# Optimization experiments

Measured on AMD Instinct MI355X. Metric: run time of the kernel, lower is better.

Reference implementation:

```python
import math
import jax, jax.numpy as jnp
import numpy as np

B, T, C = 2, 2048, 1024
H = 16
HD = C // H
WIN = 33
HALF = WIN // 2
CAUSAL = True
RADIUS, OMEGA, KSPR, STEP = 6.0, 1.0, 1.0, 0.1
EPS = 1e-8


def _spiral_step(x):
    # x: (..., 3) — the stacked (q, k, v) axis; D=3 -> rotate (x0, x1) pair.
    r = jnp.maximum(jnp.linalg.norm(x, axis=-1, keepdims=True), EPS)
    radial = (RADIUS - r) * (x / r)
    c = jnp.float32(math.cos(OMEGA * STEP))
    s = jnp.float32(math.sin(OMEGA * STEP))
    xi, xj, xl = x[..., 0], x[..., 1], x[..., 2]
    y = jnp.stack([c * xi - s * xj, s * xi + c * xj, xl], axis=-1)
    return x + STEP * (y - x + KSPR * radial)


def setup_inputs() -> dict:
    key = jax.random.key(0)
    ks = jax.random.split(key, 3)
    x = jax.random.normal(ks[0], (B, T, C), dtype=jnp.float32)
    W_attn = jax.random.normal(ks[1], (C, 3 * C), dtype=jnp.float32) * (1.0 / math.sqrt(C))
    W_proj = jax.random.normal(ks[2], (C, C), dtype=jnp.float32) * (1.0 / math.sqrt(C))
    sinks = jnp.zeros((H,), dtype=jnp.float32)
    ln_scale = jnp.ones((1,), dtype=jnp.float32) * 0.9
    ln_delta = jnp.ones((C,), dtype=jnp.float32)
    ln_bias = jnp.zeros((C,), dtype=jnp.float32)
    return {"x": x, "W_attn": W_attn, "W_proj": W_proj, "sinks": sinks,
            "ln_scale": ln_scale, "ln_delta": ln_delta, "ln_bias": ln_bias}


def reference(x, W_attn, W_proj, sinks, ln_scale, ln_delta, ln_bias):
    qkv = x @ W_attn                              # (B,T,3C)
    q, k, v = jnp.split(qkv, 3, axis=-1)          # each (B,T,C)

    # SpiralMix over the stacked (q,k,v) axis, loop_iters=2. Only q,k are
    # taken from the mixed output (v stays the pre-spiral value), matching src.
    s = jnp.stack([q, k, v], axis=-1)             # (B,T,C,3)
    s = _spiral_step(_spiral_step(s))
    q, k = s[..., 0], s[..., 1]

    def to_heads(t):
        return t.reshape(B, T, H, HD).transpose(0, 2, 1, 3)  # (B,H,T,hd)
    q, k, v = to_heads(q), to_heads(k), to_heads(v)

    # local window index
    t_idx = jnp.arange(T)
    offs = jnp.arange(-HALF, HALF + 1)
    neigh = t_idx[:, None] + offs[None, :]                    # (T,W)
    valid = (neigh >= 0) & (neigh < T)
    if CAUSAL:
        valid &= neigh <= t_idx[:, None]
    neigh_c = jnp.clip(neigh, 0, T - 1)

    k_n = k[:, :, neigh_c, :]                                 # (B,H,T,W,hd)
    v_n = v[:, :, neigh_c, :]

    inv_sqrt_d = 1.0 / math.sqrt(HD)
    scores = jnp.einsum('bhtd,bhtwd->bhtw',
                        q.astype(jnp.float32), k_n.astype(jnp.float32)) * inv_sqrt_d
    scores = jnp.where(valid[None, None], scores, -jnp.inf)

    # softmax with learned sink logits per head
    sinks_b = sinks.reshape(1, H, 1, 1).astype(scores.dtype)
    m = jnp.max(scores, axis=-1, keepdims=True)
    mj = jnp.maximum(m, sinks_b)
    exp_s = jnp.exp(scores - mj)
    denom = jnp.sum(exp_s, axis=-1, keepdims=True) + jnp.exp(sinks_b - mj)
    att = exp_s / denom                                       # (B,H,T,W)

    y = jnp.einsum('bhtw,bhtwd->bhtd', att, v_n.astype(att.dtype))
    y = y.transpose(0, 2, 1, 3).reshape(B, T, C).astype(x.dtype)
    y = y @ W_proj
    y = jnp.tanh(ln_scale * y)
    return ln_delta * y + ln_bias
```

## Files before the change

kernel.cpp:

```cpp
#include <hip/hip_runtime.h>
#include <hip/hip_fp16.h>
#include <math.h>

#define T_DIM 2048
#define B_DIM 2
#define C_DIM 1024
#define H_DIM 16
#define M_DIM 4096

typedef _Float16 f16x8 __attribute__((ext_vector_type(8)));
typedef _Float16 f16x4 __attribute__((ext_vector_type(4)));
typedef _Float16 f16x2 __attribute__((ext_vector_type(2)));
typedef float    f32x4 __attribute__((ext_vector_type(4)));

union f16x8_u { f16x8 v; f16x2 h[4]; _Float16 e[8]; };

#if defined(__has_builtin)
#  if __has_builtin(__builtin_amdgcn_fdot2)
#    define HAVE_FDOT2 1
#  endif
#endif

static __device__ __forceinline__ float FDOT2(f16x2 a, f16x2 b, float c)
{
#ifdef HAVE_FDOT2
    return __builtin_amdgcn_fdot2(a, b, c, false);
#else
    return c + (float)a[0] * (float)b[0] + (float)a[1] * (float)b[1];
#endif
}

#define ASYNC_COPY16(gsrc, ldst) \
  __builtin_amdgcn_global_load_lds( \
    (__attribute__((address_space(1))) unsigned int*)(gsrc), \
    (__attribute__((address_space(3))) unsigned int*)(ldst), 16, 0, 0)


__global__ __launch_bounds__(256) void prep_xpack_kernel(const float* __restrict__ x,
                                                         _Float16* __restrict__ xpack)
{
    __shared__ __attribute__((aligned(16))) _Float16 rows[16 * 1032];
    const int g = blockIdx.x;
    const int tid = threadIdx.x;
    const int row = tid >> 4, c16 = tid & 15;
#pragma unroll
    for (int it = 0; it < 16; ++it) {
        const int c4 = (c16 + it * 16) << 2;
        float4 v = *(const float4*)&x[(long)(g * 16 + row) * 1024 + c4];
        f16x4 o;
        o[0] = (_Float16)v.x; o[1] = (_Float16)v.y;
        o[2] = (_Float16)v.z; o[3] = (_Float16)v.w;
        *(f16x4*)&rows[row * 1032 + c4] = o;
    }
    __syncthreads();
    const int l = tid & 63, ksb = tid >> 6;
#pragma unroll
    for (int cc = 0; cc < 8; ++cc) {
        const int ks = ksb + cc * 4;
        f16x8 c = *(const f16x8*)&rows[(l & 15) * 1032 + ks * 32 + ((l >> 4) << 3)];
        *(f16x8*)&xpack[((long)(g * 32 + ks)) * 512 + l * 8] = c;
    }
}

__global__ __launch_bounds__(256) void prep_wapack_kernel(const float* __restrict__ W,
                                                          _Float16* __restrict__ wpack)
{
    __shared__ float tile[32][33];
    const int b = blockIdx.x;
    const int bk = b & 31;
    const int bn = b >> 5;
    const int tid = threadIdx.x;
    const int tx = tid & 31, ty = tid >> 5;
    const int N = 3072;
#pragma unroll
    for (int r = ty; r < 32; r += 8)
        tile[r][tx] = W[(long)(bk * 32 + r) * N + bn * 32 + tx];
    __syncthreads();
    if (tid < 128) {
        const int hh = tid >> 6, l = tid & 63;
        const int kb = (l >> 4) << 3;
        f16x8_u o;
#pragma unroll
        for (int j = 0; j < 8; ++j)
            o.e[j] = (_Float16)tile[kb + j][hh * 16 + (l & 15)];
        *(f16x8*)&wpack[((long)((bn * 2 + hh) * 32 + bk)) * 512 + l * 8] = o.v;
    }
}

__global__ __launch_bounds__(256) void prep_wpt_kernel(const float* __restrict__ W,
                                                       _Float16* __restrict__ WT)
{
    __shared__ float tile[32][33];
    const int N = 1024, K = 1024;
    const int bk = blockIdx.x & 31;
    const int bn = blockIdx.x >> 5;
    const int tx = threadIdx.x & 31, ty = threadIdx.x >> 5;
#pragma unroll
    for (int r = ty; r < 32; r += 8)
        tile[r][tx] = W[(long)(bk * 32 + r) * N + bn * 32 + tx];
    __syncthreads();
#pragma unroll
    for (int r = ty; r < 32; r += 8)
        WT[(long)(bn * 32 + r) * K + bk * 32 + tx] = (_Float16)tile[tx][r];
}

__global__ __launch_bounds__(256) void gemm1_stream_kernel(const _Float16* __restrict__ Apack,
                                                           const _Float16* __restrict__ Bpack,
                                                           _Float16* __restrict__ C)
{
    const int lane = threadIdx.x & 63;
    const int wid  = threadIdx.x >> 6;
    const int bid = ((int)blockIdx.x & 7) * 96 + ((int)blockIdx.x >> 3);
    const int mw = bid & 63;
    const int nw = (bid >> 6) * 4 + wid;

    const _Float16* abase = Apack + ((long)(mw * 4) * 32) * 512 + lane * 8;
    const _Float16* bbase = Bpack + ((long)(nw * 4) * 32) * 512 + lane * 8;

    f32x4 acc[4][4] = {};

#pragma unroll 2
    for (int t = 0; t < 32; ++t) {
        f16x8 af[4], bf[4];
#pragma unroll
        for (int i = 0; i < 4; i++) af[i] = *(const f16x8*)(abase + (i * 32 + t) * 512);
#pragma unroll
        for (int j = 0; j < 4; j++) bf[j] = *(const f16x8*)(bbase + (j * 32 + t) * 512);
#pragma unroll
        for (int i = 0; i < 4; i++)
#pragma unroll
            for (int j = 0; j < 4; j++)
                acc[i][j] = __builtin_amdgcn_mfma_f32_16x16x32_f16(af[i], bf[j], acc[i][j], 0, 0, 0);
    }

    const int fr = lane & 15;
    const int rsub = (lane >> 4) << 2;
#pragma unroll
    for (int j = 0; j < 4; j++) {
        const int col = nw * 64 + j * 16 + fr;
#pragma unroll
        for (int i = 0; i < 4; i++) {
            const int rbase = mw * 64 + i * 16 + rsub;
#pragma unroll
            for (int r = 0; r < 4; r++)
                C[(long)(rbase + r) * 3072 + col] = (_Float16)acc[i][j][r];
        }
    }
}

template<int BM>
__global__ __launch_bounds__(256) void gemm2_kernel(
    const _Float16* __restrict__ A, const _Float16* __restrict__ Bt,
    float* __restrict__ Cv, int M, int N, int K,
    const float* __restrict__ ln_scale, const float* __restrict__ ln_delta,
    const float* __restrict__ ln_bias)
{
    constexpr int M_REP   = BM / 32;
    constexpr int A_LOADS = BM / 64;
    constexpr int LPT     = A_LOADS + 2;
    __shared__ __attribute__((aligned(16))) _Float16 As[3][BM * 32];
    __shared__ __attribute__((aligned(16))) _Float16 Bs[3][128 * 32];

    const int tid  = threadIdx.x;
    const int lane = tid & 63;
    const int wave = tid >> 6;
    const int wr = wave >> 1, wc = wave & 1;

    const int nwg = gridDim.x;
    const int q8  = nwg >> 3;
    const int bid = ((int)blockIdx.x & 7) * q8 + ((int)blockIdx.x >> 3);

    const int ntn = N >> 7;
    const int m0 = (bid / ntn) * BM;
    const int n0 = (bid % ntn) << 7;

    f32x4 acc[M_REP][4] = {};

    const int ea   = tid * 8;
    const int erow = ea >> 5;
    const int xm   = ((erow & 2) << 3) | ((erow & 4) << 1);
    const int ecs  = (ea & 31) ^ xm;
    const _Float16* aptr[A_LOADS];
    const _Float16* bptr[2];
#pragma unroll
    for (int l = 0; l < A_LOADS; ++l)
        aptr[l] = A + (long)(m0 + erow + l * 64) * K + ecs;
#pragma unroll
    for (int l = 0; l < 2; ++l)
        bptr[l] = Bt + (long)(n0 + erow + l * 64) * K + ecs;

    const int fr = lane & 15;
    const int kb = (lane >> 4) << 3;
    const int xr = ((fr & 2) << 3) | ((fr & 4) << 1);
    const int kbs = kb ^ xr;
    const int NT = K >> 5;

    auto stage = [&](int tile, int slot) {
        const int k0 = tile << 5;
#pragma unroll
        for (int l = 0; l < A_LOADS; ++l) ASYNC_COPY16(aptr[l] + k0, &As[slot][ea + l * 2048]);
#pragma unroll
        for (int l = 0; l < 2; ++l)       ASYNC_COPY16(bptr[l] + k0, &Bs[slot][ea + l * 2048]);
    };

    stage(0, 0);
    stage(1, 1);

    int s = 0;
    for (int t = 0; t < NT; ++t) {
        if (t + 2 < NT) {
            int s2 = s + 2; if (s2 >= 3) s2 -= 3;
            stage(t + 2, s2);
        }
        const int rem = NT - 1 - t;
        if (rem >= 2)      asm volatile("s_waitcnt vmcnt(6)" ::: "memory");
        else if (rem == 1) asm volatile("s_waitcnt vmcnt(3)" ::: "memory");
        else               asm volatile("s_waitcnt vmcnt(0)" ::: "memory");
        __syncthreads();

        f16x8 af[M_REP], bf[4];
#pragma unroll
        for (int i = 0; i < M_REP; i++)
            af[i] = *(const f16x8*)&As[s][((wr * (BM / 2) + (i << 4) + fr) << 5) + kbs];
#pragma unroll
        for (int j = 0; j < 4; j++)
            bf[j] = *(const f16x8*)&Bs[s][(((wc << 6) + (j << 4) + fr) << 5) + kbs];
        __builtin_amdgcn_s_setprio(1);
#pragma unroll
        for (int i = 0; i < M_REP; i++)
#pragma unroll
            for (int j = 0; j < 4; j++)
                acc[i][j] = __builtin_amdgcn_mfma_f32_16x16x32_f16(af[i], bf[j], acc[i][j], 0, 0, 0);
        __builtin_amdgcn_s_setprio(0);
        if (t + 1 < NT) __syncthreads();
        ++s; if (s == 3) s = 0;
    }

    const int rsub = (lane >> 4) << 2;
    const float lsc = ln_scale[0];
#pragma unroll
    for (int j = 0; j < 4; j++) {
        const int col = n0 + (wc << 6) + (j << 4) + fr;
        const float ld = ln_delta[col], lb = ln_bias[col];
#pragma unroll
        for (int i = 0; i < M_REP; i++) {
            const int rbase = m0 + wr * (BM / 2) + (i << 4) + rsub;
#pragma unroll
            for (int r = 0; r < 4; r++) {
                float v = acc[i][j][r];
                v = ld * tanhf(lsc * v) + lb;
                Cv[(long)(rbase + r) * N + col] = v;
            }
        }
    }
}

__device__ __forceinline__ void spiral2(float& xi, float& xj, float xl)
{
    const float CS = 0.9950041652780258f;
    const float SN = 0.09983341664682815f;
#pragma unroll
    for (int s = 0; s < 2; s++) {
        float r = sqrtf(xi * xi + xj * xj + xl * xl);
        r = fmaxf(r, 1e-8f);
        const float coef = (6.0f - r) / r;
        const float yi = CS * xi - SN * xj;
        const float yj = SN * xi + CS * xj;
        const float nxi = xi + 0.1f * (yi - xi + coef * xi);
        const float nxj = xj + 0.1f * (yj - xj + coef * xj);
        const float nxl = xl + 0.1f * (coef * xl);
        xi = nxi; xj = nxj; xl = nxl;
    }
}

#define TB   128
#define ROWS 144
#define LDR  72

__global__ __launch_bounds__(128) void attn_kernel(const _Float16* __restrict__ qkv,
                                                   const float* __restrict__ sinks,
                                                   _Float16* __restrict__ yh)
{
    __shared__ __attribute__((aligned(16))) _Float16 k_lds[ROWS * LDR];
    __shared__ __attribute__((aligned(16))) _Float16 v_lds[ROWS * LDR];
    __shared__ __attribute__((aligned(16))) _Float16 q_lds[TB * LDR];

    const int tid = threadIdx.x;
    const int chunk = blockIdx.x & 15;
    const int h = (blockIdx.x >> 4) & 15;
    const int b = blockIdx.x >> 8;
    const int t0 = chunk * TB;
    const long bT = (long)b * T_DIM;

    for (int s = tid; s < ROWS * 4; s += 128) {
        const int ri = s >> 2, q4 = s & 3;
        const int gr = min(max(t0 - 16 + ri, 0), T_DIM - 1);
        const _Float16* base = qkv + (bT + gr) * 3072 + (h << 6) + (q4 << 4);
        f16x8_u qa, qb, ka, kb2, va, vb;
        qa.v  = *(const f16x8*)(base);        qb.v  = *(const f16x8*)(base + 8);
        ka.v  = *(const f16x8*)(base + 1024); kb2.v = *(const f16x8*)(base + 1032);
        va.v  = *(const f16x8*)(base + 2048); vb.v  = *(const f16x8*)(base + 2056);
        float qq[16], kk[16], vv[16];
#pragma unroll
        for (int u = 0; u < 8; u++) {
            qq[u] = (float)qa.e[u]; qq[8 + u] = (float)qb.e[u];
            kk[u] = (float)ka.e[u]; kk[8 + u] = (float)kb2.e[u];
            vv[u] = (float)va.e[u]; vv[8 + u] = (float)vb.e[u];
        }
#pragma unroll
        for (int u = 0; u < 16; u++) spiral2(qq[u], kk[u], vv[u]);
        const int lbase = ri * LDR + (q4 << 4);
        f16x8_u ko0, ko1, vo0, vo1;
#pragma unroll
        for (int u = 0; u < 8; u++) {
            ko0.e[u] = (_Float16)kk[u]; ko1.e[u] = (_Float16)kk[8 + u];
            vo0.e[u] = (_Float16)vv[u]; vo1.e[u] = (_Float16)vv[8 + u];
        }
        *(f16x8*)&k_lds[lbase]     = ko0.v;
        *(f16x8*)&k_lds[lbase + 8] = ko1.v;
        *(f16x8*)&v_lds[lbase]     = vo0.v;
        *(f16x8*)&v_lds[lbase + 8] = vo1.v;
        if (ri >= 16) {
            const int qbase = (ri - 16) * LDR + (q4 << 4);
            f16x8_u qo0, qo1;
#pragma unroll
            for (int u = 0; u < 8; u++) {
                qo0.e[u] = (_Float16)(qq[u] * 0.125f);
                qo1.e[u] = (_Float16)(qq[8 + u] * 0.125f);
            }
            *(f16x8*)&q_lds[qbase]     = qo0.v;
            *(f16x8*)&q_lds[qbase + 8] = qo1.v;
        }
    }
    __syncthreads();

    f16x8_u qv[8];
#pragma unroll
    for (int u = 0; u < 8; u++) qv[u].v = *(const f16x8*)&q_lds[tid * LDR + u * 8];

    float sc[17];
#pragma unroll
    for (int j = 0; j < 17; j++) {
        const _Float16* kr = &k_lds[(tid + j) * LDR];
        float s = 0.f;
#pragma unroll
        for (int u = 0; u < 8; u++) {
            f16x8_u kx; kx.v = *(const f16x8*)&kr[u * 8];
#pragma unroll
            for (int p = 0; p < 4; p++) s = FDOT2(qv[u].h[p], kx.h[p], s);
        }
        sc[j] = s;
    }

    const int t = t0 + tid;
#pragma unroll
    for (int j = 0; j < 17; j++)
        if (j + t < 16) sc[j] = -INFINITY;
    const float sink = sinks[h];
    float m = sink;
#pragma unroll
    for (int j = 0; j < 17; j++) m = fmaxf(m, sc[j]);
    float e[17];
    float denom = expf(sink - m);
#pragma unroll
    for (int j = 0; j < 17; j++) { e[j] = expf(sc[j] - m); denom += e[j]; }
    const float rden = 1.f / denom;
#pragma unroll
    for (int j = 0; j < 17; j++) e[j] *= rden;

    float yacc[64];
#pragma unroll
    for (int d = 0; d < 64; d++) yacc[d] = 0.f;
#pragma unroll
    for (int j = 0; j < 17; j++) {
        const float a = e[j];
        const _Float16* vr = &v_lds[(tid + j) * LDR];
#pragma unroll
        for (int u = 0; u < 8; u++) {
            f16x8_u vx; vx.v = *(const f16x8*)&vr[u * 8];
#pragma unroll
            for (int z = 0; z < 8; z++) yacc[u * 8 + z] += a * (float)vx.e[z];
        }
    }

#pragma unroll
    for (int u = 0; u < 8; u++) {
        f16x8_u yo;
#pragma unroll
        for (int z = 0; z < 8; z++) yo.e[z] = (_Float16)yacc[u * 8 + z];
        *(f16x8*)&q_lds[tid * LDR + u * 8] = yo.v;
    }
    __syncthreads();
    const int ch = tid & 7, rb = tid >> 3;
#pragma unroll
    for (int pass = 0; pass < 8; ++pass) {
        const int r = pass * 16 + rb;
        *(f16x8*)(yh + (bT + t0 + r) * 1024 + (h << 6) + ch * 8) =
            *(const f16x8*)&q_lds[r * LDR + ch * 8];
    }
}

extern "C" void kernel_launch(void* const* d_in, const int* in_sizes, int n_in,
                              void* d_out, int out_size, void* d_ws, size_t ws_size,
                              hipStream_t stream)
{
    const float* x        = (const float*)d_in[0];
    const float* W_attn   = (const float*)d_in[1];
    const float* W_proj   = (const float*)d_in[2];
    const float* sinks    = (const float*)d_in[3];
    const float* ln_scale = (const float*)d_in[4];
    const float* ln_delta = (const float*)d_in[5];
    const float* ln_bias  = (const float*)d_in[6];
    float* out = (float*)d_out;

    char* ws = (char*)d_ws;
    _Float16* xpack  = (_Float16*)(ws);
    _Float16* wapack = (_Float16*)(ws + (size_t)( 8u << 20));
    _Float16* WpT    = (_Float16*)(ws + (size_t)(14u << 20));
    _Float16* qkv16  = (_Float16*)(ws + (size_t)(16u << 20));
    _Float16* yh     = (_Float16*)(ws + (size_t)(40u << 20));

    prep_xpack_kernel <<<256,  256, 0, stream>>>(x, xpack);
    prep_wapack_kernel<<<3072, 256, 0, stream>>>(W_attn, wapack);
    prep_wpt_kernel   <<<1024, 256, 0, stream>>>(W_proj, WpT);
    gemm1_stream_kernel<<<768, 256, 0, stream>>>(xpack, wapack, qkv16);
    attn_kernel<<<512, 128, 0, stream>>>(qkv16, sinks, yh);
    gemm2_kernel<64><<<64 * 8, 256, 0, stream>>>(yh, WpT, out, 4096, 1024, 1024,
                                                 ln_scale, ln_delta, ln_bias);
}
```

Before: 178.2 us.

## Merge prep kernels and restructure both GEMMs with hybrid LDS/register-streamed operands

Folds the three preprocessing kernels into one launch to cut launch overhead. GEMM1 now uses 128x128 tiles: the weight operand is staged through LDS with async copies, and the activation operand is streamed from a pre-packed layout directly into registers, double-buffered. GEMM2 swaps roles, so W_proj is pre-packed and streamed into registers while the activations go through LDS. Explicit barriers and sched_barriers plus tuned vmcnt waits are meant to overlap global loads with MFMA work. In exchange the code carries more register pressure and hand-tuned wait counts that must match the number of outstanding loads.

```diff
diff --git a/kernel.cpp b/kernel.cpp
--- a/kernel.cpp
+++ b/kernel.cpp
@@ -36,204 +36,252 @@
     (__attribute__((address_space(3))) unsigned int*)(ldst), 16, 0, 0)
 
 
-__global__ __launch_bounds__(256) void prep_xpack_kernel(const float* __restrict__ x,
-                                                         _Float16* __restrict__ xpack)
-{
-    __shared__ __attribute__((aligned(16))) _Float16 rows[16 * 1032];
-    const int g = blockIdx.x;
+__global__ __launch_bounds__(256) void prep_kernel(const float* __restrict__ x,
+                                                   const float* __restrict__ Wa,
+                                                   const float* __restrict__ Wp,
+                                                   _Float16* __restrict__ xpack,
+                                                   _Float16* __restrict__ WaT,
+                                                   _Float16* __restrict__ wppack)
+{
+    const int bid = blockIdx.x;
     const int tid = threadIdx.x;
-    const int row = tid >> 4, c16 = tid & 15;
-#pragma unroll
-    for (int it = 0; it < 16; ++it) {
-        const int c4 = (c16 + it * 16) << 2;
-        float4 v = *(const float4*)&x[(long)(g * 16 + row) * 1024 + c4];
-        f16x4 o;
-        o[0] = (_Float16)v.x; o[1] = (_Float16)v.y;
-        o[2] = (_Float16)v.z; o[3] = (_Float16)v.w;
-        *(f16x4*)&rows[row * 1032 + c4] = o;
-    }
-    __syncthreads();
-    const int l = tid & 63, ksb = tid >> 6;
-#pragma unroll
-    for (int cc = 0; cc < 8; ++cc) {
-        const int ks = ksb + cc * 4;
-        f16x8 c = *(const f16x8*)&rows[(l & 15) * 1032 + ks * 32 + ((l >> 4) << 3)];
-        *(f16x8*)&xpack[((long)(g * 32 + ks)) * 512 + l * 8] = c;
-    }
-}
-
-__global__ __launch_bounds__(256) void prep_wapack_kernel(const float* __restrict__ W,
-                                                          _Float16* __restrict__ wpack)
-{
-    __shared__ float tile[32][33];
-    const int b = blockIdx.x;
-    const int bk = b & 31;
-    const int bn = b >> 5;
-    const int tid = threadIdx.x;
-    const int tx = tid & 31, ty = tid >> 5;
-    const int N = 3072;
-#pragma unroll
-    for (int r = ty; r < 32; r += 8)
-        tile[r][tx] = W[(long)(bk * 32 + r) * N + bn * 32 + tx];
-    __syncthreads();
-    if (tid < 128) {
-        const int hh = tid >> 6, l = tid & 63;
-        const int kb = (l >> 4) << 3;
-        f16x8_u o;
-#pragma unroll
-        for (int j = 0; j < 8; ++j)
-            o.e[j] = (_Float16)tile[kb + j][hh * 16 + (l & 15)];
-        *(f16x8*)&wpack[((long)((bn * 2 + hh) * 32 + bk)) * 512 + l * 8] = o.v;
-    }
-}
-
-__global__ __launch_bounds__(256) void prep_wpt_kernel(const float* __restrict__ W,
-                                                       _Float16* __restrict__ WT)
-{
-    __shared__ float tile[32][33];
-    const int N = 1024, K = 1024;
-    const int bk = blockIdx.x & 31;
-    const int bn = blockIdx.x >> 5;
-    const int tx = threadIdx.x & 31, ty = threadIdx.x >> 5;
-#pragma unroll
-    for (int r = ty; r < 32; r += 8)
-        tile[r][tx] = W[(long)(bk * 32 + r) * N + bn * 32 + tx];
-    __syncthreads();
-#pragma unroll
-    for (int r = ty; r < 32; r += 8)
-        WT[(long)(bn * 32 + r) * K + bk * 32 + tx] = (_Float16)tile[tx][r];
-}
-
-__global__ __launch_bounds__(256) void gemm1_stream_kernel(const _Float16* __restrict__ Apack,
-                                                           const _Float16* __restrict__ Bpack,
-                                                           _Float16* __restrict__ C)
-{
-    const int lane = threadIdx.x & 63;
-    const int wid  = threadIdx.x >> 6;
-    const int bid = ((int)blockIdx.x & 7) * 96 + ((int)blockIdx.x >> 3);
-    const int mw = bid & 63;
-    const int nw = (bid >> 6) * 4 + wid;
-
-    const _Float16* abase = Apack + ((long)(mw * 4) * 32) * 512 + lane * 8;
-    const _Float16* bbase = Bpack + ((long)(nw * 4) * 32) * 512 + lane * 8;
-
-    f32x4 acc[4][4] = {};
-
-#pragma unroll 2
-    for (int t = 0; t < 32; ++t) {
-        f16x8 af[4], bf[4];
-#pragma unroll
-        for (int i = 0; i < 4; i++) af[i] = *(const f16x8*)(abase + (i * 32 + t) * 512);
-#pragma unroll
-        for (int j = 0; j < 4; j++) bf[j] = *(const f16x8*)(bbase + (j * 32 + t) * 512);
-#pragma unroll
-        for (int i = 0; i < 4; i++)
-#pragma unroll
-            for (int j = 0; j < 4; j++)
-                acc[i][j] = __builtin_amdgcn_mfma_f32_16x16x32_f16(af[i], bf[j], acc[i][j], 0, 0, 0);
-    }
-
-    const int fr = lane & 15;
-    const int rsub = (lane >> 4) << 2;
-#pragma unroll
-    for (int j = 0; j < 4; j++) {
-        const int col = nw * 64 + j * 16 + fr;
-#pragma unroll
-        for (int i = 0; i < 4; i++) {
-            const int rbase = mw * 64 + i * 16 + rsub;
-#pragma unroll
-            for (int r = 0; r < 4; r++)
-                C[(long)(rbase + r) * 3072 + col] = (_Float16)acc[i][j][r];
-        }
-    }
-}
-
-template<int BM>
-__global__ __launch_bounds__(256) void gemm2_kernel(
-    const _Float16* __restrict__ A, const _Float16* __restrict__ Bt,
-    float* __restrict__ Cv, int M, int N, int K,
-    const float* __restrict__ ln_scale, const float* __restrict__ ln_delta,
-    const float* __restrict__ ln_bias)
-{
-    constexpr int M_REP   = BM / 32;
-    constexpr int A_LOADS = BM / 64;
-    constexpr int LPT     = A_LOADS + 2;
-    __shared__ __attribute__((aligned(16))) _Float16 As[3][BM * 32];
+    if (bid < 256) {
+        __shared__ __attribute__((aligned(16))) _Float16 rows[16 * 1032];
+        const int g = bid;
+        const int row = tid >> 4, c16 = tid & 15;
+#pragma unroll
+        for (int it = 0; it < 16; ++it) {
+            const int c4 = (c16 + it * 16) << 2;
+            float4 v = *(const float4*)&x[(long)(g * 16 + row) * 1024 + c4];
+            f16x4 o;
+            o[0] = (_Float16)v.x; o[1] = (_Float16)v.y;
+            o[2] = (_Float16)v.z; o[3] = (_Float16)v.w;
+            *(f16x4*)&rows[row * 1032 + c4] = o;
+        }
+        __syncthreads();
+        const int l = tid & 63, ksb = tid >> 6;
+#pragma unroll
+        for (int cc = 0; cc < 8; ++cc) {
+            const int ks = ksb + cc * 4;
+            f16x8 c = *(const f16x8*)&rows[(l & 15) * 1032 + ks * 32 + ((l >> 4) << 3)];
+            *(f16x8*)&xpack[((long)(g * 32 + ks)) * 512 + l * 8] = c;
+        }
+        return;
+    }
+    if (bid < 3328) {
+        __shared__ float tile[32][33];
+        const int b = bid - 256;
+        const int bk = b & 31, bn = b >> 5;
+        const int tx = tid & 31, ty = tid >> 5;
+        const int N = 3072, K = 1024;
+#pragma unroll
+        for (int r = ty; r < 32; r += 8)
+            tile[r][tx] = Wa[(long)(bk * 32 + r) * N + bn * 32 + tx];
+        __syncthreads();
+#pragma unroll
+        for (int r = ty; r < 32; r += 8)
+            WaT[(long)(bn * 32 + r) * K + bk * 32 + tx] = (_Float16)tile[tx][r];
+        return;
+    }
+    {
+        __shared__ float tile[32][33];
+        const int b = bid - 3328;
+        const int bk = b & 31, bn = b >> 5;
+        const int tx = tid & 31, ty = tid >> 5;
+        const int N = 1024;
+#pragma unroll
+        for (int r = ty; r < 32; r += 8)
+            tile[r][tx] = Wp[(long)(bk * 32 + r) * N + bn * 32 + tx];
+        __syncthreads();
+        if (tid < 128) {
+            const int hh = tid >> 6, l = tid & 63;
+            const int kb = (l >> 4) << 3;
+            f16x8_u o;
+#pragma unroll
+            for (int j = 0; j < 8; ++j)
+                o.e[j] = (_Float16)tile[kb + j][hh * 16 + (l & 15)];
+            *(f16x8*)&wppack[((long)((bn * 2 + hh) * 32 + bk)) * 512 + l * 8] = o.v;
+        }
+    }
+}
+
+__global__ __launch_bounds__(256) void gemm1_kernel(const _Float16* __restrict__ Apack,
+                                                    const _Float16* __restrict__ Bt,
+                                                    _Float16* __restrict__ C)
+{
     __shared__ __attribute__((aligned(16))) _Float16 Bs[3][128 * 32];
 
     const int tid  = threadIdx.x;
     const int lane = tid & 63;
     const int wave = tid >> 6;
     const int wr = wave >> 1, wc = wave & 1;
-
-    const int nwg = gridDim.x;
-    const int q8  = nwg >> 3;
-    const int bid = ((int)blockIdx.x & 7) * q8 + ((int)blockIdx.x >> 3);
-
-    const int ntn = N >> 7;
-    const int m0 = (bid / ntn) * BM;
-    const int n0 = (bid % ntn) << 7;
-
-    f32x4 acc[M_REP][4] = {};
+    const int K = 1024, N = 3072;
+
+    const int bid = ((int)blockIdx.x & 7) * 96 + ((int)blockIdx.x >> 3);
+    const int m0 = (bid / 24) << 7;
+    const int n0 = (bid % 24) << 7;
+
+    f32x4 acc[4][4] = {};
 
     const int ea   = tid * 8;
     const int erow = ea >> 5;
     const int xm   = ((erow & 2) << 3) | ((erow & 4) << 1);
     const int ecs  = (ea & 31) ^ xm;
-    const _Float16* aptr[A_LOADS];
-    const _Float16* bptr[2];
-#pragma unroll
-    for (int l = 0; l < A_LOADS; ++l)
-        aptr[l] = A + (long)(m0 + erow + l * 64) * K + ecs;
-#pragma unroll
-    for (int l = 0; l < 2; ++l)
-        bptr[l] = Bt + (long)(n0 + erow + l * 64) * K + ecs;
+    const _Float16* bptr0 = Bt + (long)(n0 + erow) * K + ecs;
+    const _Float16* bptr1 = Bt + (long)(n0 + erow + 64) * K + ecs;
 
     const int fr = lane & 15;
     const int kb = (lane >> 4) << 3;
     const int xr = ((fr & 2) << 3) | ((fr & 4) << 1);
     const int kbs = kb ^ xr;
-    const int NT = K >> 5;
-
-    auto stage = [&](int tile, int slot) {
-        const int k0 = tile << 5;
-#pragma unroll
-        for (int l = 0; l < A_LOADS; ++l) ASYNC_COPY16(aptr[l] + k0, &As[slot][ea + l * 2048]);
-#pragma unroll
-        for (int l = 0; l < 2; ++l)       ASYNC_COPY16(bptr[l] + k0, &Bs[slot][ea + l * 2048]);
-    };
-
-    stage(0, 0);
-    stage(1, 1);
-
-    int s = 0;
-    for (int t = 0; t < NT; ++t) {
-        if (t + 2 < NT) {
+
+    const _Float16* abase = Apack + ((long)((m0 >> 4) + wr * 4) * 32) * 512 + lane * 8;
+
+#define G1_STAGE(tile, slot) do { \
+        ASYNC_COPY16(bptr0 + ((tile) << 5), &Bs[slot][ea]); \
+        ASYNC_COPY16(bptr1 + ((tile) << 5), &Bs[slot][ea + 2048]); } while (0)
+#define G1_LOADA(dst, t) do { \
+        dst[0] = *(const f16x8*)(abase + ((0 * 32 + (t)) * 512)); \
+        dst[1] = *(const f16x8*)(abase + ((1 * 32 + (t)) * 512)); \
+        dst[2] = *(const f16x8*)(abase + ((2 * 32 + (t)) * 512)); \
+        dst[3] = *(const f16x8*)(abase + ((3 * 32 + (t)) * 512)); } while (0)
+
+    f16x8 afA[4], afB[4];
+    G1_STAGE(0, 0);
+    G1_STAGE(1, 1);
+    G1_LOADA(afA, 0);
+
+#define G1_BODY(t, CUR, NXT, slot, slot2) do { \
+        if ((t) + 1 < 32) G1_LOADA(NXT, (t) + 1); \
+        if ((t) + 2 < 32) G1_STAGE((t) + 2, slot2); \
+        const int rem = 31 - (t); \
+        if (rem >= 2)      asm volatile("s_waitcnt vmcnt(8)" ::: "memory"); \
+        else if (rem == 1) asm volatile("s_waitcnt vmcnt(6)" ::: "memory"); \
+        else               asm volatile("s_waitcnt vmcnt(0)" ::: "memory"); \
+        __builtin_amdgcn_s_barrier(); \
+        __builtin_amdgcn_sched_barrier(0); \
+        f16x8 bf[4]; \
+        _Pragma("unroll") \
+        for (int j = 0; j < 4; j++) \
+            bf[j] = *(const f16x8*)&Bs[slot][(((wc << 6) + (j << 4) + fr) << 5) + kbs]; \
+        __builtin_amdgcn_s_setprio(1); \
+        _Pragma("unroll") \
+        for (int i = 0; i < 4; i++) \
+            _Pragma("unroll") \
+            for (int j = 0; j < 4; j++) \
+                acc[i][j] = __builtin_amdgcn_mfma_f32_16x16x32_f16(CUR[i], bf[j], acc[i][j], 0, 0, 0); \
+        __builtin_amdgcn_s_setprio(0); \
+        __builtin_amdgcn_s_barrier(); \
+        __builtin_amdgcn_sched_barrier(0); } while (0)
+
+    {
+        int s = 0;
+#pragma unroll 1
+        for (int t = 0; t < 32; t += 2) {
+            int s1 = s + 1; if (s1 >= 3) s1 -= 3;
             int s2 = s + 2; if (s2 >= 3) s2 -= 3;
-            stage(t + 2, s2);
-        }
-        const int rem = NT - 1 - t;
-        if (rem >= 2)      asm volatile("s_waitcnt vmcnt(6)" ::: "memory");
-        else if (rem == 1) asm volatile("s_waitcnt vmcnt(3)" ::: "memory");
-        else               asm volatile("s_waitcnt vmcnt(0)" ::: "memory");
-        __syncthreads();
-
-        f16x8 af[M_REP], bf[4];
-#pragma unroll
-        for (int i = 0; i < M_REP; i++)
-            af[i] = *(const f16x8*)&As[s][((wr * (BM / 2) + (i << 4) + fr) << 5) + kbs];
-#pragma unroll
-        for (int j = 0; j < 4; j++)
-            bf[j] = *(const f16x8*)&Bs[s][(((wc << 6) + (j << 4) + fr) << 5) + kbs];
-        __builtin_amdgcn_s_setprio(1);
-#pragma unroll
-        for (int i = 0; i < M_REP; i++)
-#pragma unroll
-            for (int j = 0; j < 4; j++)
-                acc[i][j] = __builtin_amdgcn_mfma_f32_16x16x32_f16(af[i], bf[j], acc[i][j], 0, 0, 0);
-        __builtin_amdgcn_s_setprio(0);
-        if (t + 1 < NT) __syncthreads();
-        ++s; if (s == 3) s = 0;
+            G1_BODY(t,     afA, afB, s,  s2);
+            G1_BODY(t + 1, afB, afA, s1, s);
+            s = s2;
+        }
+    }
+
+    const int rsub = (lane >> 4) << 2;
+#pragma unroll
+    for (int j = 0; j < 4; j++) {
+        const int col = n0 + (wc << 6) + (j << 4) + fr;
+#pragma unroll
+        for (int i = 0; i < 4; i++) {
+            const int rbase = m0 + (wr << 6) + (i << 4) + rsub;
+#pragma unroll
+            for (int r = 0; r < 4; r++)
+                C[(long)(rbase + r) * N + col] = (_Float16)acc[i][j][r];
+        }
+    }
+#undef G1_STAGE
+#undef G1_LOADA
+#undef G1_BODY
+}
+
+__global__ __launch_bounds__(256) void gemm2_kernel(const _Float16* __restrict__ A,
+                                                    const _Float16* __restrict__ Bpack,
+                                                    float* __restrict__ Cv,
+                                                    const float* __restrict__ ln_scale,
+                                                    const float* __restrict__ ln_delta,
+                                                    const float* __restrict__ ln_bias)
+{
+    __shared__ __attribute__((aligned(16))) _Float16 As[3][64 * 32];
+
+    const int tid  = threadIdx.x;
+    const int lane = tid & 63;
+    const int wave = tid >> 6;
+    const int wr = wave >> 1, wc = wave & 1;
+    const int K = 1024, N = 1024;
+
+    const int bid = ((int)blockIdx.x & 7) * 64 + ((int)blockIdx.x >> 3);
+    const int m0 = (bid >> 3) << 6;
+    const int n0 = (bid & 7) << 7;
+
+    f32x4 acc[2][4] = {};
+
+    const int ea   = tid * 8;
+    const int erow = ea >> 5;
+    const int xm   = ((erow & 2) << 3) | ((erow & 4) << 1);
+    const int ecs  = (ea & 31) ^ xm;
+    const _Float16* aptr = A + (long)(m0 + erow) * K + ecs;
+
+    const int fr = lane & 15;
+    const int kb = (lane >> 4) << 3;
+    const int xr = ((fr & 2) << 3) | ((fr & 4) << 1);
+    const int kbs = kb ^ xr;
+
+    const _Float16* bbase = Bpack + ((long)((n0 >> 4) + wc * 4) * 32) * 512 + lane * 8;
+
+#define G2_STAGE(tile, slot) ASYNC_COPY16(aptr + ((tile) << 5), &As[slot][ea])
+#define G2_LOADB(dst, t) do { \
+        dst[0] = *(const f16x8*)(bbase + ((0 * 32 + (t)) * 512)); \
+        dst[1] = *(const f16x8*)(bbase + ((1 * 32 + (t)) * 512)); \
+        dst[2] = *(const f16x8*)(bbase + ((2 * 32 + (t)) * 512)); \
+        dst[3] = *(const f16x8*)(bbase + ((3 * 32 + (t)) * 512)); } while (0)
+
+    f16x8 bfA[4], bfB[4];
+    G2_STAGE(0, 0);
+    G2_STAGE(1, 1);
+    G2_LOADB(bfA, 0);
+
+#define G2_BODY(t, CUR, NXT, slot, slot2) do { \
+        if ((t) + 1 < 32) G2_LOADB(NXT, (t) + 1); \
+        if ((t) + 2 < 32) G2_STAGE((t) + 2, slot2); \
+        const int rem = 31 - (t); \
+        if (rem >= 2)      asm volatile("s_waitcnt vmcnt(10)" ::: "memory"); \
+        else if (rem == 1) asm volatile("s_waitcnt vmcnt(9)" ::: "memory"); \
+        else               asm volatile("s_waitcnt vmcnt(0)" ::: "memory"); \
+        __builtin_amdgcn_s_barrier(); \
+        __builtin_amdgcn_sched_barrier(0); \
+        f16x8 af[2]; \
+        _Pragma("unroll") \
+        for (int i = 0; i < 2; i++) \
+            af[i] = *(const f16x8*)&As[slot][(((wr << 5) + (i << 4) + fr) << 5) + kbs]; \
+        __builtin_amdgcn_s_setprio(1); \
+        _Pragma("unroll") \
+        for (int i = 0; i < 2; i++) \
+            _Pragma("unroll") \
+            for (int j = 0; j < 4; j++) \
+                acc[i][j] = __builtin_amdgcn_mfma_f32_16x16x32_f16(af[i], CUR[j], acc[i][j], 0, 0, 0); \
+        __builtin_amdgcn_s_setprio(0); \
+        __builtin_amdgcn_s_barrier(); \
+        __builtin_amdgcn_sched_barrier(0); } while (0)
+
+    {
+        int s = 0;
+#pragma unroll 1
+        for (int t = 0; t < 32; t += 2) {
+            int s1 = s + 1; if (s1 >= 3) s1 -= 3;
+            int s2 = s + 2; if (s2 >= 3) s2 -= 3;
+            G2_BODY(t,     bfA, bfB, s,  s2);
+            G2_BODY(t + 1, bfB, bfA, s1, s);
+            s = s2;
+        }
     }
 
     const int rsub = (lane >> 4) << 2;
@@ -243,16 +291,18 @@
         const int col = n0 + (wc << 6) + (j << 4) + fr;
         const float ld = ln_delta[col], lb = ln_bias[col];
 #pragma unroll
-        for (int i = 0; i < M_REP; i++) {
-            const int rbase = m0 + wr * (BM / 2) + (i << 4) + rsub;
+        for (int i = 0; i < 2; i++) {
+            const int rbase = m0 + (wr << 5) + (i << 4) + rsub;
 #pragma unroll
             for (int r = 0; r < 4; r++) {
                 float v = acc[i][j][r];
-                v = ld * tanhf(lsc * v) + lb;
-                Cv[(long)(rbase + r) * N + col] = v;
+                Cv[(long)(rbase + r) * N + col] = ld * tanhf(lsc * v) + lb;
             }
         }
     }
+#undef G2_STAGE
+#undef G2_LOADB
+#undef G2_BODY
 }
 
 __device__ __forceinline__ void spiral2(float& xi, float& xj, float xl)
@@ -415,16 +465,13 @@
 
     char* ws = (char*)d_ws;
     _Float16* xpack  = (_Float16*)(ws);
-    _Float16* wapack = (_Float16*)(ws + (size_t)( 8u << 20));
-    _Float16* WpT    = (_Float16*)(ws + (size_t)(14u << 20));
+    _Float16* WaT    = (_Float16*)(ws + (size_t)( 8u << 20));
+    _Float16* wppack = (_Float16*)(ws + (size_t)(14u << 20));
     _Float16* qkv16  = (_Float16*)(ws + (size_t)(16u << 20));
     _Float16* yh     = (_Float16*)(ws + (size_t)(40u << 20));
 
-    prep_xpack_kernel <<<256,  256, 0, stream>>>(x, xpack);
-    prep_wapack_kernel<<<3072, 256, 0, stream>>>(W_attn, wapack);
-    prep_wpt_kernel   <<<1024, 256, 0, stream>>>(W_proj, WpT);
-    gemm1_stream_kernel<<<768, 256, 0, stream>>>(xpack, wapack, qkv16);
+    prep_kernel<<<4352, 256, 0, stream>>>(x, W_attn, W_proj, xpack, WaT, wppack);
+    gemm1_kernel<<<768, 256, 0, stream>>>(xpack, WaT, qkv16);
     attn_kernel<<<512, 128, 0, stream>>>(qkv16, sinks, yh);
-    gemm2_kernel<64><<<64 * 8, 256, 0, stream>>>(yh, WpT, out, 4096, 1024, 1024,
-                                                 ln_scale, ln_delta, ln_bias);
-}
+    gemm2_kernel<<<512, 256, 0, stream>>>(yh, wppack, out, ln_scale, ln_delta, ln_bias);
+}
```

Result: no change. 176.5 us (-0.9%).
